# Performance work log

Measured on AMD Instinct MI355X. Metric: run time of the kernel, lower is better.

The kernel has to match this reference:

```python
import jax, jax.numpy as jnp
import numpy as np

NHEAD = 8

def layernorm(x, w, b, eps=1e-5):
    mu = jnp.mean(x, axis=-1, keepdims=True)
    var = jnp.mean((x - mu) ** 2, axis=-1, keepdims=True)
    return (x - mu) * jax.lax.rsqrt(var + eps) * w + b

def setup_inputs() -> dict:
    key = jax.random.key(0)
    ks = jax.random.split(key, 3)
    N, in_dim, dim = 2048, 256, 256
    point = jax.random.normal(ks[0], (N, in_dim), dtype=jnp.float32)
    w_qkv = jax.random.normal(ks[1], (in_dim, 3 * dim), dtype=jnp.float32) * (in_dim ** -0.5)
    w_proj = jax.random.normal(ks[2], (dim, dim), dtype=jnp.float32) * (dim ** -0.5)
    return {
        "point": point,
        "w_qkv": w_qkv,
        "w_proj": w_proj,
        "b_proj": jnp.zeros((dim,), jnp.float32),
        "norm1_w": jnp.ones((in_dim,), jnp.float32),
        "norm1_b": jnp.zeros((in_dim,), jnp.float32),
        "norm2_w": jnp.ones((dim,), jnp.float32),
        "norm2_b": jnp.zeros((dim,), jnp.float32),
        "topk": 16,
    }

def reference(point, w_qkv, w_proj, b_proj, norm1_w, norm1_b, norm2_w, norm2_b, topk):
    # Coarse level of QTAttB (i == 0, ONE_BATCH=True)
    N, in_dim = point.shape
    dim = w_proj.shape[0]
    Ch = dim // NHEAD  # per-head channels
    x = layernorm(point, norm1_w, norm1_b)[None]            # [1, N, in_dim]
    qkv = (x @ w_qkv).reshape(1, N, 3, NHEAD, Ch)
    q, k, v = qkv[:, :, 0], qkv[:, :, 1], qkv[:, :, 2]      # [1, N, H, Ch]
    # QK: nlhd,nshd->nlsh ; softmax over key axis s (dim=-2 in torch = axis 2)
    QK = jnp.einsum('blhd,bshd->blsh', q, k)                # [1, N, N, H]
    A = jax.nn.softmax(QK * (Ch ** -0.5), axis=2)
    A_mean = jnp.mean(A, axis=-1)                           # [1, N, N]
    _, topk_idx = jax.lax.top_k(A_mean, topk)               # [1, N, topk]
    message = jnp.einsum('blsh,bshd->blhd', A, v).reshape(1, N, dim)
    message = message @ w_proj + b_proj
    message = v.reshape(1, N, dim) + message
    message = message[0]                                    # squeeze batch
    out = layernorm(message, norm2_w, norm2_b)              # final_message = norm2(message)
    return out, topk_idx[0]
```

## Files before the change

### kernel.cpp

```cpp
#include <hip/hip_runtime.h>

#define NTOK   2048
#define DIM    256
#define NH     8
#define CH     32
#define QB     16
#define TOPK_K 16
#define SCALE  0.17677669529663687f
#define LN_EPS 1e-5f

#define PBL    260
#define PBH    (QB * PBL)
#define PSCALE 16384.f
#define RPSCALE (1.f / 16384.f)

typedef _Float16 h16;
typedef _Float16 h16x8 __attribute__((ext_vector_type(8)));
typedef float    f32x4 __attribute__((ext_vector_type(4)));

#define MFMA16(a, b, c) __builtin_amdgcn_mfma_f32_16x16x32_f16((a), (b), (c), 0, 0, 0)


template<int NT>
__device__ __forceinline__ float block_sum(float v, float* red){
  #pragma unroll
  for (int off = 32; off > 0; off >>= 1) v += __shfl_xor(v, off, 64);
  const int t = threadIdx.x;
  if ((t & 63) == 0) red[t >> 6] = v;
  __syncthreads();
  float s = 0.f;
  #pragma unroll
  for (int w = 0; w < NT/64; w++) s += red[w];
  __syncthreads();
  return s;
}

__global__ __launch_bounds__(256) void reorder_w_kernel(
    const float* __restrict__ src_qkv, const float* __restrict__ src_proj,
    h16* __restrict__ WF, h16* __restrict__ WP)
{
  const int b = blockIdx.x;
  const float* src; h16* dst; int ld, pair;
  if (b < 96){ src = src_qkv;  dst = WF; ld = 768; pair = b * 4 + (threadIdx.x >> 6); }
  else       { src = src_proj; dst = WP; ld = 256; pair = (b - 96) * 4 + (threadIdx.x >> 6); }
  const int l  = threadIdx.x & 63;
  const int cg = pair >> 3, ks = pair & 7;
  h16x8 hi8, lo8;
  #pragma unroll
  for (int j = 0; j < 8; j++){
    const float v = src[(size_t)(ks * 32 + (l >> 4) * 8 + j) * ld + cg * 16 + (l & 15)];
    const h16 h = (h16)v;
    hi8[j] = h;
    lo8[j] = (h16)(v - (float)h);
  }
  *(h16x8*)&dst[(size_t)((cg * 8 + ks) * 2 + 0) * 512 + l * 8] = hi8;
  *(h16x8*)&dst[(size_t)((cg * 8 + ks) * 2 + 1) * 512 + l * 8] = lo8;
}

__global__ __launch_bounds__(256) void zero2_kernel(
    float* __restrict__ a, int na, float* __restrict__ b, int nb)
{
  const int stride = gridDim.x * blockDim.x;
  for (int k = blockIdx.x * blockDim.x + threadIdx.x; k < na; k += stride) a[k] = 0.f;
  for (int k = blockIdx.x * blockDim.x + threadIdx.x; k < nb; k += stride) b[k] = 0.f;
}

__global__ __launch_bounds__(1024) void ln_qkv_kernel(
    const float* __restrict__ point,
    const h16*   __restrict__ WF,
    const float* __restrict__ c1,
    const float* __restrict__ c2,
    h16*   __restrict__ QF,
    h16*   __restrict__ KF,
    h16*   __restrict__ VF,
    float* __restrict__ V)
{
  __shared__ float xs[16][261];
  __shared__ float garr[256], barr[256];
  __shared__ float red[16];
  const int t  = threadIdx.x;
  const int wv = t >> 6;
  const int l  = t & 63;
  const int r  = l & 15;
  const int g  = l >> 4;
  const int tg = blockIdx.x >> 1;
  const int ch = blockIdx.x & 1;
  const int l0 = tg * 16;

  const float a1 = (t < 256) ? c1[t] : 0.f;
  const float a2 = (t < 256) ? c2[t] : 0.f;
  const float s1 = block_sum<1024>(fabsf(a1), red);
  const float s2 = block_sum<1024>(fabsf(a2), red);
  if (t < 256){ garr[t] = (s1 > s2) ? a1 : a2; barr[t] = (s1 > s2) ? a2 : a1; }
  __syncthreads();

  {
    const float4 x = *(const float4*)&point[(size_t)(l0 + wv) * DIM + 4 * l];
    float s = x.x + x.y + x.z + x.w;
    #pragma unroll
    for (int off = 1; off < 64; off <<= 1) s += __shfl_xor(s, off, 64);
    const float mu = s * (1.f / DIM);
    const float d0 = x.x - mu, d1 = x.y - mu, d2 = x.z - mu, d3 = x.w - mu;
    float ss = d0 * d0 + d1 * d1 + d2 * d2 + d3 * d3;
    #pragma unroll
    for (int off = 1; off < 64; off <<= 1) ss += __shfl_xor(ss, off, 64);
    const float rsd = rsqrtf(ss * (1.f / DIM) + LN_EPS);
    xs[wv][4 * l + 0] = d0 * rsd * garr[4 * l + 0] + barr[4 * l + 0];
    xs[wv][4 * l + 1] = d1 * rsd * garr[4 * l + 1] + barr[4 * l + 1];
    xs[wv][4 * l + 2] = d2 * rsd * garr[4 * l + 2] + barr[4 * l + 2];
    xs[wv][4 * l + 3] = d3 * rsd * garr[4 * l + 3] + barr[4 * l + 3];
  }
  __syncthreads();

  h16x8 ah[8], al[8];
  #pragma unroll
  for (int ks = 0; ks < 8; ks++){
    #pragma unroll
    for (int j = 0; j < 8; j++){
      const float v = xs[r][ks * 32 + 8 * g + j];
      const h16 hi = (h16)v;
      ah[ks][j] = hi;
      al[ks][j] = (h16)(v - (float)hi);
    }
  }

  const int kgb = tg;
  #pragma unroll
  for (int cgi = 0; cgi < 2; cgi++){
    if (cgi == 1 && wv >= 8) break;
    const int cg = ch * 24 + (cgi == 0 ? wv : 16 + wv);
    f32x4 acc = {0.f, 0.f, 0.f, 0.f};
    const h16* wf = WF + (size_t)cg * 8192 + (size_t)l * 8;
    #pragma unroll
    for (int ks = 0; ks < 8; ks++){
      const h16x8 bh = *(const h16x8*)(wf + ks * 1024);
      const h16x8 bl = *(const h16x8*)(wf + ks * 1024 + 512);
      acc = MFMA16(ah[ks], bh, acc);
      acc = MFMA16(al[ks], bh, acc);
      acc = MFMA16(ah[ks], bl, acc);
    }
    const int typ = cg >> 4;
    const int c0  = (cg & 15) * 16 + r;
    #pragma unroll
    for (int q4 = 0; q4 < 4; q4++){
      const int tok = 4 * g + q4;
      if (typ == 0){
        const float qs = acc[q4] * SCALE;
        const h16 qhi = (h16)qs;
        const int wq = c0 >> 5, gq = (c0 & 31) >> 3, jq = c0 & 7;
        const size_t qidx = (((size_t)(tg * 8 + wq) * 2 + 0) * 64 + (gq * 16 + tok)) * 8 + jq;
        QF[qidx]       = qhi;
        QF[qidx + 512] = (h16)(qs - (float)qhi);
      } else if (typ == 1){
        const int wh = c0 >> 5, gp = (c0 & 31) >> 3, jj = c0 & 7;
        const float kv = acc[q4];
        const h16 kh2 = (h16)kv;
        const size_t kidx = (size_t)(wh * 128 + kgb) * 1024
                          + (size_t)(gp * 16 + tok) * 8 + jj;
        KF[kidx]       = kh2;
        KF[kidx + 512] = (h16)(kv - (float)kh2);
      } else {
        V[(size_t)(l0 + tok) * DIM + c0] = acc[q4];
        const int wh = c0 >> 5, hh = (c0 & 31) >> 4, cp = c0 & 15;
        const int key = l0 + tok;
        const int kb = key >> 5, krem = key & 31, gpp = krem >> 3, jpp = krem & 7;
        VF[(size_t)((wh * 64 + kb) * 2 + hh) * 512
           + (size_t)(gpp * 16 + cp) * 8 + jpp] = (h16)acc[q4];
      }
    }
  }
}

__global__ __launch_bounds__(1024) void z_kernel(
    const h16* __restrict__ QF,
    const h16* __restrict__ KF,
    float*     __restrict__ Zp)
{
  const int t  = threadIdx.x;
  const int wv = t >> 6;
  const int w  = wv & 7;
  const int sh = wv >> 3;
  const int l  = t & 63;
  const int r  = l & 15;
  const int g  = l >> 4;
  const int tg = blockIdx.x >> 1;
  const int hb = blockIdx.x & 1;

  const h16* qf = QF + ((size_t)(tg * 8 + w) * 2) * 512 + (size_t)l * 8;
  const h16x8 qh = *(const h16x8*)(qf);
  const h16x8 ql = *(const h16x8*)(qf + 512);

  const h16* kf = KF + (size_t)(w * 128 + hb * 64 + sh * 32) * 1024 + (size_t)l * 8;
  float zs[4] = {0.f, 0.f, 0.f, 0.f};
  #pragma unroll 2
  for (int kgi = 0; kgi < 32; kgi++){
    const h16x8 bh = *(const h16x8*)(kf + (size_t)kgi * 1024);
    const h16x8 bl = *(const h16x8*)(kf + (size_t)kgi * 1024 + 512);
    f32x4 d = {0.f, 0.f, 0.f, 0.f};
    d = MFMA16(qh, bh, d);
    d = MFMA16(ql, bh, d);
    d = MFMA16(qh, bl, d);
    #pragma unroll
    for (int q4 = 0; q4 < 4; q4++) zs[q4] += __expf(d[q4]);
  }
  #pragma unroll
  for (int q4 = 0; q4 < 4; q4++){
    #pragma unroll
    for (int off = 1; off < 16; off <<= 1) zs[q4] += __shfl_xor(zs[q4], off, 64);
  }
  if (r == 0){
    #pragma unroll
    for (int q4 = 0; q4 < 4; q4++)
      atomicAdd(&Zp[(size_t)w * NTOK + tg * 16 + 4 * g + q4], zs[q4]);
  }
}

__global__ __launch_bounds__(1024) __attribute__((amdgpu_waves_per_eu(4)))
void attn_fused_kernel(
    const h16*   __restrict__ QF,
    const h16*   __restrict__ KF,
    const h16*   __restrict__ VF,
    const float* __restrict__ Zp,
    float*       __restrict__ msgacc,
    float2*      __restrict__ candG)
{
  __shared__ float pbuf[NH * PBH];
  __shared__ float cand_v[16][64];
  __shared__ float cand_i[16][64];
  __shared__ float zbuf[NH][QB];

  const int t  = threadIdx.x;
  const int wv = t >> 6;
  const int w  = wv & 7;
  const int hf = wv >> 3;
  const int l  = t & 63;
  const int r  = l & 15;
  const int g  = l >> 4;
  const int qt = blockIdx.x >> 1;
  const int hb = blockIdx.x & 1;
  const int l0 = qt * 16;

  const h16* qf = QF + ((size_t)(qt * 8 + w) * 2) * 512 + (size_t)l * 8;
  const h16x8 qh = *(const h16x8*)(qf);
  const h16x8 ql = *(const h16x8*)(qf + 512);

  if (t < 128) zbuf[t >> 4][t & 15] = Zp[(size_t)(t >> 4) * NTOK + l0 + (t & 15)];
  __syncthreads();
  float rZ[4];
  #pragma unroll
  for (int q4 = 0; q4 < 4; q4++) rZ[q4] = 1.f / zbuf[w][4 * g + q4];

  const h16* kfw = KF + (size_t)(w * 128 + hb * 64) * 1024 + (size_t)l * 8;
  const h16* vfw = VF + (size_t)(w * 64 + hb * 32) * 1024 + (size_t)l * 8;

  f32x4 macc[2];
  #pragma unroll
  for (int dg = 0; dg < 2; dg++) macc[dg] = (f32x4){0.f, 0.f, 0.f, 0.f};

  for (int ti = 0; ti < 4; ti++){
    const h16* vft = vfw + (size_t)((ti * 8 + hf * 4) * 2) * 512;

    h16x8 pva[4], pvb[4];
    pva[0] = *(const h16x8*)(vft);
    pvb[0] = *(const h16x8*)(vft + 512);
    pva[1] = *(const h16x8*)(vft + 1024);
    pvb[1] = *(const h16x8*)(vft + 1024 + 512);

    {
      const h16* kft = kfw + (size_t)(ti * 16 + hf * 8) * 1024;
      #pragma unroll 2
      for (int kgi = 0; kgi < 8; kgi++){
        const h16x8 bh = *(const h16x8*)(kft + (size_t)kgi * 1024);
        const h16x8 bl = *(const h16x8*)(kft + (size_t)kgi * 1024 + 512);
        f32x4 d = {0.f, 0.f, 0.f, 0.f};
        d = MFMA16(qh, bh, d);
        d = MFMA16(ql, bh, d);
        d = MFMA16(qh, bl, d);
        const int kbr = hf * 128 + kgi * 16 + r;
        pbuf[w * PBH + (4 * g + 0) * PBL + kbr] = __expf(d[0]) * rZ[0];
        pbuf[w * PBH + (4 * g + 1) * PBL + kbr] = __expf(d[1]) * rZ[1];
        pbuf[w * PBH + (4 * g + 2) * PBL + kbr] = __expf(d[2]) * rZ[2];
        pbuf[w * PBH + (4 * g + 3) * PBL + kbr] = __expf(d[3]) * rZ[3];
      }
    }
    __syncthreads();

    pva[2] = *(const h16x8*)(vft + 2048);
    pvb[2] = *(const h16x8*)(vft + 2048 + 512);
    pva[3] = *(const h16x8*)(vft + 3072);
    pvb[3] = *(const h16x8*)(vft + 3072 + 512);

    #pragma unroll
    for (int st = 0; st < 4; st++){
      h16x8 pa;
      const float* pp = &pbuf[w * PBH + r * PBL + hf * 128 + st * 32 + 8 * g];
      const float4 p0 = *(const float4*)pp;
      const float4 p1 = *(const float4*)(pp + 4);
      pa[0] = (h16)(p0.x * PSCALE); pa[1] = (h16)(p0.y * PSCALE);
      pa[2] = (h16)(p0.z * PSCALE); pa[3] = (h16)(p0.w * PSCALE);
      pa[4] = (h16)(p1.x * PSCALE); pa[5] = (h16)(p1.y * PSCALE);
      pa[6] = (h16)(p1.z * PSCALE); pa[7] = (h16)(p1.w * PSCALE);
      macc[0] = MFMA16(pa, pva[st], macc[0]);
      macc[1] = MFMA16(pa, pvb[st], macc[1]);
    }

    {
      float4 su = make_float4(0.f, 0.f, 0.f, 0.f);
      #pragma unroll
      for (int hh = 0; hh < 8; hh++){
        const float4 v = *(const float4*)&pbuf[hh * PBH + wv * PBL + 4 * l];
        su.x += v.x; su.y += v.y; su.z += v.z; su.w += v.w;
      }
      float v0 = su.x * 0.125f, v1 = su.y * 0.125f;
      float v2 = su.z * 0.125f, v3 = su.w * 0.125f;
      const int base = hb * 1024 + ti * 256 + 4 * l;
      #pragma unroll
      for (int it = 0; it < 16; it++){
        float bv = v0; int bj = 0;
        if (v1 > bv){ bv = v1; bj = 1; }
        if (v2 > bv){ bv = v2; bj = 2; }
        if (v3 > bv){ bv = v3; bj = 3; }
        int bi = base + bj;
        #pragma unroll
        for (int off = 1; off < 64; off <<= 1){
          const float ov = __shfl_xor(bv, off, 64);
          const int   oi = __shfl_xor(bi, off, 64);
          if (ov > bv || (ov == bv && oi < bi)){ bv = ov; bi = oi; }
        }
        if (l == 0){ cand_v[wv][ti * 16 + it] = bv; cand_i[wv][ti * 16 + it] = (float)bi; }
        const int dj = bi - base;
        if (dj >= 0 && dj < 4){
          if      (dj == 0) v0 = -1e30f;
          else if (dj == 1) v1 = -1e30f;
          else if (dj == 2) v2 = -1e30f;
          else              v3 = -1e30f;
        }
      }
    }
    __syncthreads();
  }

  {
    float mv = cand_v[wv][l];
    float mi = cand_i[wv][l];
    #pragma unroll
    for (int it = 0; it < 16; it++){
      float bv = mv, bi = mi;
      #pragma unroll
      for (int off = 1; off < 64; off <<= 1){
        const float ov = __shfl_xor(bv, off, 64);
        const float oi = __shfl_xor(bi, off, 64);
        if (ov > bv || (ov == bv && oi < bi)){ bv = ov; bi = oi; }
      }
      if (l == 0){
        float2 c; c.x = bv; c.y = bi;
        candG[((size_t)(l0 + wv) * 2 + hb) * 16 + it] = c;
      }
      if (mi == bi) mv = -1e30f;
    }
  }

  float* msg_s = pbuf;
  #pragma unroll
  for (int dg = 0; dg < 2; dg++)
    #pragma unroll
    for (int q4 = 0; q4 < 4; q4++)
      msg_s[(hf * 16 + 4 * g + q4) * PBL + w * CH + dg * 16 + r] = macc[dg][q4] * RPSCALE;
  __syncthreads();
  #pragma unroll
  for (int k2 = 0; k2 < 4; k2++){
    const int cell = t + 1024 * k2;
    const int q = cell >> 8, d = cell & 255;
    const float val = msg_s[(q) * PBL + d] + msg_s[(16 + q) * PBL + d];
    atomicAdd(&msgacc[(size_t)(l0 + q) * DIM + d], val);
  }
}

__global__ __launch_bounds__(1024) void topk_kernel(
    const float2* __restrict__ candG, float* __restrict__ out_idx)
{
  const int wv = threadIdx.x >> 6, l = threadIdx.x & 63;
  const int row = blockIdx.x * 16 + wv;
  float v = -1e30f, fi = 1e9f;
  if (l < 32){
    const float2 p = candG[(size_t)row * 32 + l];
    v = p.x; fi = p.y;
  }
  #pragma unroll
  for (int it = 0; it < TOPK_K; it++){
    float bv = v, bi = fi;
    #pragma unroll
    for (int off = 1; off < 64; off <<= 1){
      const float ov = __shfl_xor(bv, off, 64);
      const float oi = __shfl_xor(bi, off, 64);
      if (ov > bv || (ov == bv && oi < bi)){ bv = ov; bi = oi; }
    }
    if (l == 0) out_idx[(size_t)row * TOPK_K + it] = bi;
    if (fi == bi) v = -1e30f;
  }
}

__global__ __launch_bounds__(1024) void proj_ln_kernel(
    const float* __restrict__ msg,
    const float* __restrict__ V,
    const h16*   __restrict__ WP,
    const float* __restrict__ b_proj,
    const float* __restrict__ c1,
    const float* __restrict__ c2,
    float* __restrict__ out)
{
  __shared__ float xs[16][261];
  __shared__ float ms2[16][261];
  __shared__ float garr[256], barr[256], bparr[256];
  __shared__ float red[16];
  const int t  = threadIdx.x;
  const int wv = t >> 6;
  const int l  = t & 63;
  const int r  = l & 15;
  const int g  = l >> 4;
  const int l0 = blockIdx.x * 16;

  const float a1 = (t < 256) ? c1[t] : 0.f;
  const float a2 = (t < 256) ? c2[t] : 0.f;
  const float s1 = block_sum<1024>(fabsf(a1), red);
  const float s2 = block_sum<1024>(fabsf(a2), red);
  if (t < 256){
    garr[t]  = (s1 > s2) ? a1 : a2;
    barr[t]  = (s1 > s2) ? a2 : a1;
    bparr[t] = b_proj[t];
  }

  {
    const float4 x = *(const float4*)&msg[(size_t)(l0 + wv) * DIM + 4 * l];
    xs[wv][4 * l + 0] = x.x; xs[wv][4 * l + 1] = x.y;
    xs[wv][4 * l + 2] = x.z; xs[wv][4 * l + 3] = x.w;
  }
  __syncthreads();

  h16x8 ah[8], al[8];
  #pragma unroll
  for (int ks = 0; ks < 8; ks++){
    #pragma unroll
    for (int j = 0; j < 8; j++){
      const float v = xs[r][ks * 32 + 8 * g + j];
      const h16 hi = (h16)v;
      ah[ks][j] = hi;
      al[ks][j] = (h16)(v - (float)hi);
    }
  }

  f32x4 acc = {0.f, 0.f, 0.f, 0.f};
  {
    const h16* wp = WP + (size_t)wv * 8192 + (size_t)l * 8;
    #pragma unroll
    for (int ks = 0; ks < 8; ks++){
      const h16x8 bh = *(const h16x8*)(wp + ks * 1024);
      const h16x8 bl = *(const h16x8*)(wp + ks * 1024 + 512);
      acc = MFMA16(ah[ks], bh, acc);
      acc = MFMA16(al[ks], bh, acc);
      acc = MFMA16(ah[ks], bl, acc);
    }
  }

  const int dc = wv * 16 + r;
  #pragma unroll
  for (int q4 = 0; q4 < 4; q4++){
    const int tok = 4 * g + q4;
    ms2[tok][dc] = acc[q4] + bparr[dc] + V[(size_t)(l0 + tok) * DIM + dc];
  }
  __syncthreads();

  {
    const float x0 = ms2[wv][4 * l + 0], x1 = ms2[wv][4 * l + 1];
    const float x2 = ms2[wv][4 * l + 2], x3 = ms2[wv][4 * l + 3];
    float s = x0 + x1 + x2 + x3;
    #pragma unroll
    for (int off = 1; off < 64; off <<= 1) s += __shfl_xor(s, off, 64);
    const float mu = s * (1.f / DIM);
    const float d0 = x0 - mu, d1 = x1 - mu, d2 = x2 - mu, d3 = x3 - mu;
    float ss = d0 * d0 + d1 * d1 + d2 * d2 + d3 * d3;
    #pragma unroll
    for (int off = 1; off < 64; off <<= 1) ss += __shfl_xor(ss, off, 64);
    const float rsd = rsqrtf(ss * (1.f / DIM) + LN_EPS);
    float4 o;
    o.x = d0 * rsd * garr[4 * l + 0] + barr[4 * l + 0];
    o.y = d1 * rsd * garr[4 * l + 1] + barr[4 * l + 1];
    o.z = d2 * rsd * garr[4 * l + 2] + barr[4 * l + 2];
    o.w = d3 * rsd * garr[4 * l + 3] + barr[4 * l + 3];
    *(float4*)&out[(size_t)(l0 + wv) * DIM + 4 * l] = o;
  }
}

extern "C" void kernel_launch(void* const* d_in, const int* in_sizes, int n_in,
                              void* d_out, int out_size, void* d_ws, size_t ws_size,
                              hipStream_t stream) {
  const float* point  = nullptr;
  const float* w_qkv  = nullptr;
  const float* w_proj = nullptr;
  const float* v256[5] = {nullptr, nullptr, nullptr, nullptr, nullptr};
  int n256 = 0;
  for (int i = 0; i < n_in; i++){
    const int sz = in_sizes[i];
    if      (sz == NTOK * DIM)      point  = (const float*)d_in[i];
    else if (sz == DIM * 3 * DIM)   w_qkv  = (const float*)d_in[i];
    else if (sz == DIM * DIM)       w_proj = (const float*)d_in[i];
    else if (sz == DIM && n256 < 5) v256[n256++] = (const float*)d_in[i];
  }
  const float* b_proj = v256[0];
  const float* n1a    = v256[1];
  const float* n1c    = v256[2];
  const float* n2a    = v256[3];
  const float* n2c    = v256[4];

  float* out     = (float*)d_out;
  float* out_idx = out + (size_t)NTOK * DIM;

  char* ws = (char*)d_ws;
  h16*   QF  = (h16*)  (ws);
  float* V   = (float*)(ws + ((size_t)2 << 20));
  h16*   KF  = (h16*)  (ws + ((size_t)4 << 20));
  h16*   VF  = (h16*)  (ws + ((size_t)6 << 20));
  h16*   WF  = (h16*)  (ws + ((size_t)7 << 20));
  h16*   WP  = (h16*)  (ws + ((size_t)7 << 20) + 786432);
  float2* candG = (float2*)(ws + ((size_t)7 << 20));
  float*  Zp    = (float*) (ws + ((size_t)7 << 20) + 524288);
  float*  msgacc = out;

  reorder_w_kernel <<<128, 256,  0, stream>>>(w_qkv, w_proj, WF, WP);
  ln_qkv_kernel    <<<256, 1024, 0, stream>>>(point, WF, n1a, n1c, QF, KF, VF, V);
  zero2_kernel     <<<512, 256,  0, stream>>>(msgacc, NTOK * DIM, Zp, NH * NTOK);
  z_kernel         <<<256, 1024, 0, stream>>>(QF, KF, Zp);
  attn_fused_kernel<<<256, 1024, 0, stream>>>(QF, KF, VF, Zp, msgacc, candG);
  topk_kernel      <<<128, 1024, 0, stream>>>(candG, out_idx);
  proj_ln_kernel   <<<128, 1024, 0, stream>>>(msgacc, V, WP, b_proj, n2a, n2c, out);
}
```

Before: 198.6 us.

## Split attention key range into quarters and move Q splitting into consumers

The fused attention kernel now splits each query tile's key range four ways instead of two. This doubles the grid to 512 blocks and halves the per-block LDS probability buffer, which should allow more resident blocks and better load balance. Q is written as plain fp32, and each consumer kernel builds the fp16 hi/lo split itself. Top-k candidates are stored as separate value and uint16 index arrays, and Zp now lives in the out_idx region. The cost is twice as many atomic adds into the message accumulator and more candidates for the final top-k kernel to merge.

```diff
diff --git a/kernel.cpp b/kernel.cpp
--- a/kernel.cpp
+++ b/kernel.cpp
@@ -4,13 +4,12 @@
 #define DIM    256
 #define NH     8
 #define CH     32
-#define QB     16
 #define TOPK_K 16
 #define SCALE  0.17677669529663687f
 #define LN_EPS 1e-5f
 
-#define PBL    260
-#define PBH    (QB * PBL)
+#define PBL2   132
+#define PBH2   (16 * PBL2)
 #define PSCALE 16384.f
 #define RPSCALE (1.f / 16384.f)
 
@@ -70,7 +69,7 @@
     const h16*   __restrict__ WF,
     const float* __restrict__ c1,
     const float* __restrict__ c2,
-    h16*   __restrict__ QF,
+    float* __restrict__ Q,
     h16*   __restrict__ KF,
     h16*   __restrict__ VF,
     float* __restrict__ V)
@@ -145,12 +144,7 @@
     for (int q4 = 0; q4 < 4; q4++){
       const int tok = 4 * g + q4;
       if (typ == 0){
-        const float qs = acc[q4] * SCALE;
-        const h16 qhi = (h16)qs;
-        const int wq = c0 >> 5, gq = (c0 & 31) >> 3, jq = c0 & 7;
-        const size_t qidx = (((size_t)(tg * 8 + wq) * 2 + 0) * 64 + (gq * 16 + tok)) * 8 + jq;
-        QF[qidx]       = qhi;
-        QF[qidx + 512] = (h16)(qs - (float)qhi);
+        Q[(size_t)(l0 + tok) * DIM + c0] = acc[q4];
       } else if (typ == 1){
         const int wh = c0 >> 5, gp = (c0 & 31) >> 3, jj = c0 & 7;
         const float kv = acc[q4];
@@ -172,9 +166,9 @@
 }
 
 __global__ __launch_bounds__(1024) void z_kernel(
-    const h16* __restrict__ QF,
-    const h16* __restrict__ KF,
-    float*     __restrict__ Zp)
+    const float* __restrict__ Q,
+    const h16*   __restrict__ KF,
+    float*       __restrict__ Zp)
 {
   const int t  = threadIdx.x;
   const int wv = t >> 6;
@@ -186,9 +180,20 @@
   const int tg = blockIdx.x >> 1;
   const int hb = blockIdx.x & 1;
 
-  const h16* qf = QF + ((size_t)(tg * 8 + w) * 2) * 512 + (size_t)l * 8;
-  const h16x8 qh = *(const h16x8*)(qf);
-  const h16x8 ql = *(const h16x8*)(qf + 512);
+  h16x8 qh, ql;
+  {
+    const float* qp = &Q[(size_t)(tg * 16 + r) * DIM + w * CH + 8 * g];
+    const float4 q0 = *(const float4*)qp;
+    const float4 q1 = *(const float4*)(qp + 4);
+    const float qv[8] = {q0.x, q0.y, q0.z, q0.w, q1.x, q1.y, q1.z, q1.w};
+    #pragma unroll
+    for (int j = 0; j < 8; j++){
+      const float s = qv[j] * SCALE;
+      const h16 hi = (h16)s;
+      qh[j] = hi;
+      ql[j] = (h16)(s - (float)hi);
+    }
+  }
 
   const h16* kf = KF + (size_t)(w * 128 + hb * 64 + sh * 32) * 1024 + (size_t)l * 8;
   float zs[4] = {0.f, 0.f, 0.f, 0.f};
@@ -217,32 +222,44 @@
 
 __global__ __launch_bounds__(1024) __attribute__((amdgpu_waves_per_eu(4)))
 void attn_fused_kernel(
-    const h16*   __restrict__ QF,
+    const float* __restrict__ Q,
     const h16*   __restrict__ KF,
     const h16*   __restrict__ VF,
     const float* __restrict__ Zp,
     float*       __restrict__ msgacc,
-    float2*      __restrict__ candG)
-{
-  __shared__ float pbuf[NH * PBH];
+    float*       __restrict__ candV,
+    unsigned short* __restrict__ candI)
+{
+  __shared__ float pbuf[NH * PBH2];
   __shared__ float cand_v[16][64];
   __shared__ float cand_i[16][64];
-  __shared__ float zbuf[NH][QB];
+  __shared__ float zbuf[NH][16];
 
   const int t  = threadIdx.x;
   const int wv = t >> 6;
   const int w  = wv & 7;
-  const int hf = wv >> 3;
+  const int sh = wv >> 3;
   const int l  = t & 63;
   const int r  = l & 15;
   const int g  = l >> 4;
-  const int qt = blockIdx.x >> 1;
-  const int hb = blockIdx.x & 1;
+  const int qt = blockIdx.x >> 2;
+  const int kq = blockIdx.x & 3;
   const int l0 = qt * 16;
 
-  const h16* qf = QF + ((size_t)(qt * 8 + w) * 2) * 512 + (size_t)l * 8;
-  const h16x8 qh = *(const h16x8*)(qf);
-  const h16x8 ql = *(const h16x8*)(qf + 512);
+  h16x8 qh, ql;
+  {
+    const float* qp = &Q[(size_t)(l0 + r) * DIM + w * CH + 8 * g];
+    const float4 q0 = *(const float4*)qp;
+    const float4 q1 = *(const float4*)(qp + 4);
+    const float qv[8] = {q0.x, q0.y, q0.z, q0.w, q1.x, q1.y, q1.z, q1.w};
+    #pragma unroll
+    for (int j = 0; j < 8; j++){
+      const float s = qv[j] * SCALE;
+      const h16 hi = (h16)s;
+      qh[j] = hi;
+      ql[j] = (h16)(s - (float)hi);
+    }
+  }
 
   if (t < 128) zbuf[t >> 4][t & 15] = Zp[(size_t)(t >> 4) * NTOK + l0 + (t & 15)];
   __syncthreads();
@@ -250,77 +267,67 @@
   #pragma unroll
   for (int q4 = 0; q4 < 4; q4++) rZ[q4] = 1.f / zbuf[w][4 * g + q4];
 
-  const h16* kfw = KF + (size_t)(w * 128 + hb * 64) * 1024 + (size_t)l * 8;
-  const h16* vfw = VF + (size_t)(w * 64 + hb * 32) * 1024 + (size_t)l * 8;
+  const h16* kfw = KF + (size_t)(w * 128 + kq * 32) * 1024 + (size_t)l * 8;
 
   f32x4 macc[2];
   #pragma unroll
   for (int dg = 0; dg < 2; dg++) macc[dg] = (f32x4){0.f, 0.f, 0.f, 0.f};
 
   for (int ti = 0; ti < 4; ti++){
-    const h16* vft = vfw + (size_t)((ti * 8 + hf * 4) * 2) * 512;
-
-    h16x8 pva[4], pvb[4];
-    pva[0] = *(const h16x8*)(vft);
-    pvb[0] = *(const h16x8*)(vft + 512);
-    pva[1] = *(const h16x8*)(vft + 1024);
-    pvb[1] = *(const h16x8*)(vft + 1024 + 512);
+    const size_t vbase = ((size_t)(w * 64 + kq * 16 + ti * 4 + sh * 2) * 2) * 512
+                       + (size_t)l * 8;
+    const h16x8 pv00 = *(const h16x8*)(VF + vbase);
+    const h16x8 pv01 = *(const h16x8*)(VF + vbase + 512);
+    const h16x8 pv10 = *(const h16x8*)(VF + vbase + 1024);
+    const h16x8 pv11 = *(const h16x8*)(VF + vbase + 1536);
 
     {
-      const h16* kft = kfw + (size_t)(ti * 16 + hf * 8) * 1024;
-      #pragma unroll 2
-      for (int kgi = 0; kgi < 8; kgi++){
+      const h16* kft = kfw + (size_t)(ti * 8 + sh * 4) * 1024;
+      #pragma unroll
+      for (int kgi = 0; kgi < 4; kgi++){
         const h16x8 bh = *(const h16x8*)(kft + (size_t)kgi * 1024);
         const h16x8 bl = *(const h16x8*)(kft + (size_t)kgi * 1024 + 512);
         f32x4 d = {0.f, 0.f, 0.f, 0.f};
         d = MFMA16(qh, bh, d);
         d = MFMA16(ql, bh, d);
         d = MFMA16(qh, bl, d);
-        const int kbr = hf * 128 + kgi * 16 + r;
-        pbuf[w * PBH + (4 * g + 0) * PBL + kbr] = __expf(d[0]) * rZ[0];
-        pbuf[w * PBH + (4 * g + 1) * PBL + kbr] = __expf(d[1]) * rZ[1];
-        pbuf[w * PBH + (4 * g + 2) * PBL + kbr] = __expf(d[2]) * rZ[2];
-        pbuf[w * PBH + (4 * g + 3) * PBL + kbr] = __expf(d[3]) * rZ[3];
+        const int kbr = sh * 64 + kgi * 16 + r;
+        pbuf[w * PBH2 + (4 * g + 0) * PBL2 + kbr] = __expf(d[0]) * rZ[0];
+        pbuf[w * PBH2 + (4 * g + 1) * PBL2 + kbr] = __expf(d[1]) * rZ[1];
+        pbuf[w * PBH2 + (4 * g + 2) * PBL2 + kbr] = __expf(d[2]) * rZ[2];
+        pbuf[w * PBH2 + (4 * g + 3) * PBL2 + kbr] = __expf(d[3]) * rZ[3];
       }
     }
     __syncthreads();
 
-    pva[2] = *(const h16x8*)(vft + 2048);
-    pvb[2] = *(const h16x8*)(vft + 2048 + 512);
-    pva[3] = *(const h16x8*)(vft + 3072);
-    pvb[3] = *(const h16x8*)(vft + 3072 + 512);
-
-    #pragma unroll
-    for (int st = 0; st < 4; st++){
+    #pragma unroll
+    for (int st = 0; st < 2; st++){
       h16x8 pa;
-      const float* pp = &pbuf[w * PBH + r * PBL + hf * 128 + st * 32 + 8 * g];
+      const float* pp = &pbuf[w * PBH2 + r * PBL2 + sh * 64 + st * 32 + 8 * g];
       const float4 p0 = *(const float4*)pp;
       const float4 p1 = *(const float4*)(pp + 4);
       pa[0] = (h16)(p0.x * PSCALE); pa[1] = (h16)(p0.y * PSCALE);
       pa[2] = (h16)(p0.z * PSCALE); pa[3] = (h16)(p0.w * PSCALE);
       pa[4] = (h16)(p1.x * PSCALE); pa[5] = (h16)(p1.y * PSCALE);
       pa[6] = (h16)(p1.z * PSCALE); pa[7] = (h16)(p1.w * PSCALE);
-      macc[0] = MFMA16(pa, pva[st], macc[0]);
-      macc[1] = MFMA16(pa, pvb[st], macc[1]);
+      macc[0] = MFMA16(pa, st == 0 ? pv00 : pv10, macc[0]);
+      macc[1] = MFMA16(pa, st == 0 ? pv01 : pv11, macc[1]);
     }
 
     {
-      float4 su = make_float4(0.f, 0.f, 0.f, 0.f);
+      float am0 = 0.f, am1 = 0.f;
       #pragma unroll
       for (int hh = 0; hh < 8; hh++){
-        const float4 v = *(const float4*)&pbuf[hh * PBH + wv * PBL + 4 * l];
-        su.x += v.x; su.y += v.y; su.z += v.z; su.w += v.w;
+        am0 += pbuf[hh * PBH2 + wv * PBL2 + l];
+        am1 += pbuf[hh * PBH2 + wv * PBL2 + 64 + l];
       }
-      float v0 = su.x * 0.125f, v1 = su.y * 0.125f;
-      float v2 = su.z * 0.125f, v3 = su.w * 0.125f;
-      const int base = hb * 1024 + ti * 256 + 4 * l;
+      float v0 = am0 * 0.125f, v1 = am1 * 0.125f;
+      const int base = kq * 512 + ti * 128;
+      const int i0 = base + l, i1 = base + 64 + l;
       #pragma unroll
       for (int it = 0; it < 16; it++){
-        float bv = v0; int bj = 0;
-        if (v1 > bv){ bv = v1; bj = 1; }
-        if (v2 > bv){ bv = v2; bj = 2; }
-        if (v3 > bv){ bv = v3; bj = 3; }
-        int bi = base + bj;
+        float bv; int bi;
+        if (v0 >= v1){ bv = v0; bi = i0; } else { bv = v1; bi = i1; }
         #pragma unroll
         for (int off = 1; off < 64; off <<= 1){
           const float ov = __shfl_xor(bv, off, 64);
@@ -328,13 +335,8 @@
           if (ov > bv || (ov == bv && oi < bi)){ bv = ov; bi = oi; }
         }
         if (l == 0){ cand_v[wv][ti * 16 + it] = bv; cand_i[wv][ti * 16 + it] = (float)bi; }
-        const int dj = bi - base;
-        if (dj >= 0 && dj < 4){
-          if      (dj == 0) v0 = -1e30f;
-          else if (dj == 1) v1 = -1e30f;
-          else if (dj == 2) v2 = -1e30f;
-          else              v3 = -1e30f;
-        }
+        if      (bi == i0) v0 = -1e30f;
+        else if (bi == i1) v1 = -1e30f;
       }
     }
     __syncthreads();
@@ -353,8 +355,8 @@
         if (ov > bv || (ov == bv && oi < bi)){ bv = ov; bi = oi; }
       }
       if (l == 0){
-        float2 c; c.x = bv; c.y = bi;
-        candG[((size_t)(l0 + wv) * 2 + hb) * 16 + it] = c;
+        candV[(size_t)(l0 + wv) * 64 + kq * 16 + it] = bv;
+        candI[(size_t)(l0 + wv) * 64 + kq * 16 + it] = (unsigned short)(int)bi;
       }
       if (mi == bi) mv = -1e30f;
     }
@@ -365,27 +367,25 @@
   for (int dg = 0; dg < 2; dg++)
     #pragma unroll
     for (int q4 = 0; q4 < 4; q4++)
-      msg_s[(hf * 16 + 4 * g + q4) * PBL + w * CH + dg * 16 + r] = macc[dg][q4] * RPSCALE;
+      msg_s[(sh * 16 + 4 * g + q4) * 260 + w * CH + dg * 16 + r] = macc[dg][q4] * RPSCALE;
   __syncthreads();
   #pragma unroll
   for (int k2 = 0; k2 < 4; k2++){
     const int cell = t + 1024 * k2;
     const int q = cell >> 8, d = cell & 255;
-    const float val = msg_s[(q) * PBL + d] + msg_s[(16 + q) * PBL + d];
+    const float val = msg_s[q * 260 + d] + msg_s[(16 + q) * 260 + d];
     atomicAdd(&msgacc[(size_t)(l0 + q) * DIM + d], val);
   }
 }
 
 __global__ __launch_bounds__(1024) void topk_kernel(
-    const float2* __restrict__ candG, float* __restrict__ out_idx)
+    const float* __restrict__ candV, const unsigned short* __restrict__ candI,
+    float* __restrict__ out_idx)
 {
   const int wv = threadIdx.x >> 6, l = threadIdx.x & 63;
   const int row = blockIdx.x * 16 + wv;
-  float v = -1e30f, fi = 1e9f;
-  if (l < 32){
-    const float2 p = candG[(size_t)row * 32 + l];
-    v = p.x; fi = p.y;
-  }
+  float v  = candV[(size_t)row * 64 + l];
+  float fi = (float)candI[(size_t)row * 64 + l];
   #pragma unroll
   for (int it = 0; it < TOPK_K; it++){
     float bv = v, bi = fi;
@@ -516,21 +516,22 @@
   float* out_idx = out + (size_t)NTOK * DIM;
 
   char* ws = (char*)d_ws;
-  h16*   QF  = (h16*)  (ws);
+  float* Q   = (float*)(ws);
   float* V   = (float*)(ws + ((size_t)2 << 20));
   h16*   KF  = (h16*)  (ws + ((size_t)4 << 20));
   h16*   VF  = (h16*)  (ws + ((size_t)6 << 20));
   h16*   WF  = (h16*)  (ws + ((size_t)7 << 20));
   h16*   WP  = (h16*)  (ws + ((size_t)7 << 20) + 786432);
-  float2* candG = (float2*)(ws + ((size_t)7 << 20));
-  float*  Zp    = (float*) (ws + ((size_t)7 << 20) + 524288);
-  float*  msgacc = out;
+  float*          candV = (float*)         (ws + ((size_t)7 << 20));
+  unsigned short* candI = (unsigned short*)(ws + ((size_t)7 << 20) + 524288);
+  float* msgacc = out;
+  float* Zp     = out_idx;
 
   reorder_w_kernel <<<128, 256,  0, stream>>>(w_qkv, w_proj, WF, WP);
-  ln_qkv_kernel    <<<256, 1024, 0, stream>>>(point, WF, n1a, n1c, QF, KF, VF, V);
+  ln_qkv_kernel    <<<256, 1024, 0, stream>>>(point, WF, n1a, n1c, Q, KF, VF, V);
   zero2_kernel     <<<512, 256,  0, stream>>>(msgacc, NTOK * DIM, Zp, NH * NTOK);
-  z_kernel         <<<256, 1024, 0, stream>>>(QF, KF, Zp);
-  attn_fused_kernel<<<256, 1024, 0, stream>>>(QF, KF, VF, Zp, msgacc, candG);
-  topk_kernel      <<<128, 1024, 0, stream>>>(candG, out_idx);
+  z_kernel         <<<256, 1024, 0, stream>>>(Q, KF, Zp);
+  attn_fused_kernel<<<512, 1024, 0, stream>>>(Q, KF, VF, Zp, msgacc, candV, candI);
+  topk_kernel      <<<128, 1024, 0, stream>>>(candV, candI, out_idx);
   proj_ln_kernel   <<<128, 1024, 0, stream>>>(msgacc, V, WP, b_proj, n2a, n2c, out);
 }
```

Result: slower. 254.0 us (+27.9%).
